# Kernel optimization log

Hardware: AMD Instinct MI355X
Metric: run time of the kernel (lower is better)

## Reference

```python
import jax, jax.numpy as jnp
import numpy as np

WD, WH, WW = 2, 7, 7
N = WD * WH * WW            # 98 tokens per window
C = 192                     # dim
H = 6                       # num_heads
HD = C // H                 # head_dim = 32
NW = 512                    # number of windows per sample
B = 4                       # batch
B_ = B * NW                 # 2048 windows total
TABLE = (2 * WD - 1) * (2 * WH - 1) * (2 * WW - 1)  # 507


def _relative_position_index():
    d, h, w = np.meshgrid(np.arange(WD), np.arange(WH), np.arange(WW), indexing='ij')
    coords = np.stack([d, h, w]).reshape(3, -1)              # (3, N)
    rel = coords[:, :, None] - coords[:, None, :]            # (3, N, N)
    rel = rel.transpose(1, 2, 0).astype(np.int64)            # (N, N, 3)
    rel[:, :, 0] += WD - 1
    rel[:, :, 1] += WH - 1
    rel[:, :, 2] += WW - 1
    rel[:, :, 0] *= (2 * WH - 1) * (2 * WW - 1)
    rel[:, :, 1] *= 2 * WW - 1
    return jnp.asarray(rel.sum(-1), dtype=jnp.int32)         # (N, N)


def setup_inputs() -> dict:
    key = jax.random.key(0)
    ks = jax.random.split(key, 7)
    return {
        'x': jax.random.normal(ks[0], (B_, N, C), dtype=jnp.float32),
        'mask': jax.random.normal(ks[1], (NW, N, N), dtype=jnp.float32),
        'qkv_w': jax.random.normal(ks[2], (3 * C, C), dtype=jnp.float32) * 0.02,
        'qkv_b': jnp.zeros((3 * C,), dtype=jnp.float32),
        'proj_w': jax.random.normal(ks[3], (C, C), dtype=jnp.float32) * 0.02,
        'proj_b': jnp.zeros((C,), dtype=jnp.float32),
        'rpb_table': jax.random.normal(ks[4], (TABLE, H), dtype=jnp.float32) * 0.02,
        'rel_pos_index': _relative_position_index(),
    }


def reference(x, mask, qkv_w, qkv_b, proj_w, proj_b, rpb_table, rel_pos_index):
    Bw, n, c = x.shape
    hd = c // H
    scale = hd ** -0.5
    qkv = (x @ qkv_w.T + qkv_b).reshape(Bw, n, 3, H, hd)
    q, k, v = qkv[:, :, 0], qkv[:, :, 1], qkv[:, :, 2]       # (Bw, n, H, hd)
    # attn = (q @ k^T) * scale  (scale applied after matmul, as in source)
    attn = jnp.einsum('bihd,bjhd->bhij', q, k) * scale       # (Bw, H, n, n)
    bias = rpb_table[rel_pos_index]                          # (n, n, H)
    attn = attn + jnp.transpose(bias, (2, 0, 1))[None]       # broadcast over Bw
    nw = mask.shape[0]
    attn = attn.reshape(Bw // nw, nw, H, n, n) + mask[None, :, None]
    attn = jax.nn.softmax(attn.reshape(Bw, H, n, n), axis=-1)
    out = jnp.einsum('bhij,bjhd->bihd', attn, v).reshape(Bw, n, c)
    return out @ proj_w.T + proj_b
```

## Files before the change

### kernel.cpp

```cpp
#include <hip/hip_runtime.h>
#include <hip/hip_bf16.h>

using bf16   = __bf16;
using bf16x4 = __attribute__((ext_vector_type(4))) __bf16;
using bf16x8 = __attribute__((ext_vector_type(8))) __bf16;
using f32x4  = __attribute__((ext_vector_type(4))) float;

#define B_TOT 2048
#define NTOK  98
#define CDIM  192
#define NHEAD 6
#define HDIM  32
#define NWIN  512
#define NN    (NTOK*NTOK)
#define QKV_ELEMS ((size_t)B_TOT*NHEAD*NTOK*HDIM)
#define MROWS 200704
#define SCALE 0.17677669529663687f

#define MFMA(a,b,c) __builtin_amdgcn_mfma_f32_16x16x32_bf16((a),(b),(c),0,0,0)

#define GLD16(gp, lp) __builtin_amdgcn_global_load_lds(                        \
    (const __attribute__((address_space(1))) void*)(gp),                       \
    (__attribute__((address_space(3))) void*)(lp), 16, 0, 0)

__global__ void build_bias(const float* __restrict__ table,
                           const int* __restrict__ rel,
                           float* __restrict__ bias) {
    int t = blockIdx.x * 256 + threadIdx.x;
    if (t < NN) {
        int idx = rel[t];
        #pragma unroll
        for (int h = 0; h < NHEAD; ++h)
            bias[h * NN + t] = table[idx * NHEAD + h];
    }
}

__global__ void conv_swz(const float* __restrict__ src, bf16* __restrict__ dst,
                         int nchunk) {
    int t = blockIdx.x * 256 + threadIdx.x;
    if (t < nchunk) {
        int row = t / 24, c = t % 24;
        const float* s = src + (size_t)row * CDIM + c * 8;
        bf16x8 o;
        #pragma unroll
        for (int e = 0; e < 8; ++e) o[e] = (bf16)s[e];
        *(bf16x8*)(dst + (size_t)row * CDIM + ((c ^ (row & 7)) << 3)) = o;
    }
}

__global__ __launch_bounds__(256) void qkv_gemm(
    const float* __restrict__ x, const bf16* __restrict__ wb,
    const float* __restrict__ bvec,
    bf16* __restrict__ qdst, bf16* __restrict__ kdst, bf16* __restrict__ vdst)
{
    __shared__ char Bs[2][24576];
    const int tid = threadIdx.x, lane = tid & 63, wv = tid >> 6;
    const int l15 = lane & 15, l16 = lane >> 4;
    const int m0 = blockIdx.x * 64;

    {
        const char* bsrc = (const char*)wb;
        #pragma unroll
        for (int j = 0; j < 6; ++j) {
            const int ch = wv * 6 + j;
            GLD16(bsrc + ch * 1024 + lane * 16, Bs[0] + ch * 1024);
        }
    }

    const int arow = wv * 16 + l15;
    const int grow = m0 + arow;
    const float* xr = x + (size_t)grow * CDIM + l16 * 8;
    bf16x8 af[6];
    #pragma unroll
    for (int ks = 0; ks < 6; ++ks) {
        float4 v0 = *(const float4*)(xr + ks * 32);
        float4 v1 = *(const float4*)(xr + ks * 32 + 4);
        bf16x8 a;
        a[0] = (bf16)v0.x; a[1] = (bf16)v0.y; a[2] = (bf16)v0.z; a[3] = (bf16)v0.w;
        a[4] = (bf16)v1.x; a[5] = (bf16)v1.y; a[6] = (bf16)v1.z; a[7] = (bf16)v1.w;
        af[ks] = a;
    }

    __syncthreads();

    const int rowoff = (grow / NTOK) * 18816 + (grow % NTOK) * 32;
    const f32x4 z4 = {0.f, 0.f, 0.f, 0.f};

    #pragma unroll
    for (int nc = 0; nc < 9; ++nc) {
        if (nc < 8) {
            const char* bsrc = (const char*)wb + (size_t)(nc + 1) * 24576;
            #pragma unroll
            for (int j = 0; j < 6; ++j) {
                const int ch = wv * 6 + j;
                GLD16(bsrc + ch * 1024 + lane * 16, Bs[(nc + 1) & 1] + ch * 1024);
            }
        }

        f32x4 acc[4];
        #pragma unroll
        for (int ct = 0; ct < 4; ++ct) acc[ct] = z4;

        #pragma unroll
        for (int ks = 0; ks < 6; ++ks) {
            #pragma unroll
            for (int ct = 0; ct < 4; ++ct) {
                const int brow = ct * 16 + l15;
                bf16x8 bf = *(const bf16x8*)(Bs[nc & 1] + brow * 384
                                             + (((ks * 4 + l16) ^ (brow & 7)) << 4));
                acc[ct] = MFMA(bf, af[ks], acc[ct]);
            }
        }

        #pragma unroll
        for (int ct = 0; ct < 4; ++ct) {
            const int g0    = nc * 64 + ct * 16;
            const int which = g0 / CDIM;
            const int cm    = g0 % CDIM;
            const int h     = cm >> 5, hd0 = cm & 31;
            const float4 bvf = *(const float4*)(bvec + g0 + l16 * 4);
            bf16x4 s;
            #pragma unroll
            for (int r = 0; r < 4; ++r) {
                float v = acc[ct][r] + ((const float*)&bvf)[r];
                if (which == 0) v *= SCALE;
                s[r] = (bf16)v;
            }
            bf16* dp = (which == 0) ? qdst : (which == 1) ? kdst : vdst;
            *(bf16x4*)(dp + rowoff + h * 3136 + hd0 + l16 * 4) = s;
        }
        __syncthreads();
    }
}

__global__ __launch_bounds__(256) void attn_fused(
    const bf16* __restrict__ q, const bf16* __restrict__ k,
    const bf16* __restrict__ v,
    const float* __restrict__ mask, const float* __restrict__ bias,
    bf16* __restrict__ ao)
{
    __shared__ char lds[4 * 8192 + 4 * 4096 + 4 * 64];
    const int tid = threadIdx.x, lane = tid & 63, wv = tid >> 6;
    const int l15 = lane & 15, l16 = lane >> 4;
    char*  Vt   = lds + wv * 8192;
    char*  P    = lds + 32768 + wv * 4096;
    float* invS = (float*)(lds + 49152 + wv * 64);

    const int u = blockIdx.x * 4 + wv;
    const int b = u / NHEAD, h = u - b * NHEAD;
    const int w = b & (NWIN - 1);
    const size_t bho = (size_t)u * 3136;

    bf16x8 vvv[7];
    #pragma unroll
    for (int t = 0; t < 7; ++t) {
        int idx = t * 64 + lane;
        int n = idx >> 2; if (n > 97) n = 97;
        int hd0 = (idx & 3) * 8;
        vvv[t] = *(const bf16x8*)(v + bho + n * 32 + hd0);
    }

    bf16x8 kf[7];
    #pragma unroll
    for (int jt = 0; jt < 7; ++jt) {
        int kr = jt * 16 + l15; if (kr > 97) kr = 97;
        kf[jt] = *(const bf16x8*)(k + bho + kr * HDIM + l16 * 8);
    }

    #pragma unroll
    for (int t = 0; t < 7; ++t) {
        int idx = t * 64 + lane;
        if (idx < 392) {
            int n = idx >> 2, hd0 = (idx & 3) * 8;
            #pragma unroll
            for (int e = 0; e < 8; ++e) {
                int hd = hd0 + e;
                *(bf16*)(Vt + hd * 256 + (((n >> 3) ^ (hd & 7)) << 4) + ((n & 7) << 1))
                    = vvv[t][e];
            }
        }
    }
    #pragma unroll
    for (int t = 0; t < 15; ++t) {
        int idx = t * 64 + lane;
        int hd = idx / 30, n = 98 + idx % 30;
        *(bf16*)(Vt + hd * 256 + (((n >> 3) ^ (hd & 7)) << 4) + ((n & 7) << 1)) = (bf16)0.f;
    }
    {
        int zr = lane >> 2;
        int zc = 112 + (lane & 3) * 4;
        *(unsigned long long*)(P + zr * 256 + (((zc >> 3) ^ (zr & 7)) << 4)
                               + ((zc & 7) << 1)) = 0ull;
    }

    const float* mrow = mask + (size_t)w * NN;
    const float* brow = bias + (size_t)h * NN;
    bf16* dst = ao + (size_t)b * NTOK * CDIM;
    const f32x4 z4 = {0.f, 0.f, 0.f, 0.f};

    #pragma unroll 1
    for (int it = 0; it < 7; ++it) {
        int qrow = it * 16 + l15; if (qrow > 97) qrow = 97;
        const bf16x8 qf = *(const bf16x8*)(q + bho + qrow * HDIM + l16 * 8);
        f32x4 acc[7];
        __builtin_amdgcn_s_setprio(1);
        #pragma unroll
        for (int jt = 0; jt < 7; ++jt)
            acc[jt] = MFMA(qf, kf[jt], z4);
        __builtin_amdgcn_s_setprio(0);

        #pragma unroll
        for (int r = 0; r < 4; ++r) {
            int i = it * 16 + l16 * 4 + r; if (i > 97) i = 97;
            float s = 0.f;
            #pragma unroll
            for (int jt = 0; jt < 7; ++jt) {
                int j = jt * 16 + l15;
                float mbv = (j < NTOK) ? (mrow[i * NTOK + j] + brow[i * NTOK + j])
                                       : -__builtin_inff();
                float e = __expf(acc[jt][r] + mbv);
                acc[jt][r] = e; s += e;
            }
            s += __shfl_xor(s, 1, 16);
            s += __shfl_xor(s, 2, 16);
            s += __shfl_xor(s, 4, 16);
            s += __shfl_xor(s, 8, 16);
            if (l15 == 0) invS[l16 * 4 + r] = 1.f / s;
        }

        #pragma unroll
        for (int jt = 0; jt < 7; ++jt) {
            #pragma unroll
            for (int r = 0; r < 4; ++r) {
                int row = l16 * 4 + r;
                int j = jt * 16 + l15;
                *(bf16*)(P + row * 256 + (((j >> 3) ^ (row & 7)) << 4) + ((j & 7) << 1))
                    = (bf16)acc[jt][r];
            }
        }

        f32x4 o0 = z4, o1 = z4;
        __builtin_amdgcn_s_setprio(1);
        #pragma unroll
        for (int ks = 0; ks < 4; ++ks) {
            int kchunk = ks * 4 + l16;
            bf16x8 pf = *(const bf16x8*)(P + l15 * 256 + ((kchunk ^ (l15 & 7)) << 4));
            bf16x8 v0 = *(const bf16x8*)(Vt + l15 * 256 + ((kchunk ^ (l15 & 7)) << 4));
            bf16x8 v1 = *(const bf16x8*)(Vt + (16 + l15) * 256 + ((kchunk ^ (l15 & 7)) << 4));
            o0 = MFMA(v0, pf, o0);
            o1 = MFMA(v1, pf, o1);
        }
        __builtin_amdgcn_s_setprio(0);

        {
            int row = it * 16 + l15;
            if (row < NTOK) {
                float inv = invS[l15];
                bf16x4 s0, s1;
                #pragma unroll
                for (int r = 0; r < 4; ++r) {
                    s0[r] = (bf16)(o0[r] * inv);
                    s1[r] = (bf16)(o1[r] * inv);
                }
                const int swr = (b * NTOK + row) & 7;
                const int c0 = h * 4 + (l16 >> 1);
                const int c1 = c0 + 2;
                const int wi = (l16 & 1) << 2;
                *(bf16x4*)(dst + (size_t)row * CDIM + (((c0 ^ swr) << 3) | wi)) = s0;
                *(bf16x4*)(dst + (size_t)row * CDIM + (((c1 ^ swr) << 3) | wi)) = s1;
            }
        }
    }
}

__global__ __launch_bounds__(256) void proj_gemm(
    const bf16* __restrict__ ao, const bf16* __restrict__ wb,
    const float* __restrict__ bvec, float* __restrict__ out)
{
    __shared__ char As[24576];
    __shared__ char Bs[2][24576];
    const int tid = threadIdx.x, lane = tid & 63, wv = tid >> 6;
    const int l15 = lane & 15, l16 = lane >> 4;
    const int m0 = blockIdx.x * 64;

    {
        const char* asrc = (const char*)ao + (size_t)m0 * 384;
        const char* bsrc = (const char*)wb;
        #pragma unroll
        for (int j = 0; j < 6; ++j) {
            const int ch = wv * 6 + j;
            GLD16(asrc + ch * 1024 + lane * 16, As + ch * 1024);
            GLD16(bsrc + ch * 1024 + lane * 16, Bs[0] + ch * 1024);
        }
    }
    __syncthreads();

    const int arow = wv * 16 + l15;
    bf16x8 af[6];
    #pragma unroll
    for (int ks = 0; ks < 6; ++ks)
        af[ks] = *(const bf16x8*)(As + arow * 384 + (((ks * 4 + l16) ^ (arow & 7)) << 4));

    const size_t orow = (size_t)(m0 + arow) * CDIM;
    const f32x4 z4 = {0.f, 0.f, 0.f, 0.f};

    #pragma unroll
    for (int nc = 0; nc < 3; ++nc) {
        if (nc < 2) {
            const char* bsrc = (const char*)wb + (size_t)(nc + 1) * 24576;
            #pragma unroll
            for (int j = 0; j < 6; ++j) {
                const int ch = wv * 6 + j;
                GLD16(bsrc + ch * 1024 + lane * 16, Bs[(nc + 1) & 1] + ch * 1024);
            }
        }

        f32x4 acc[4];
        #pragma unroll
        for (int ct = 0; ct < 4; ++ct) acc[ct] = z4;

        #pragma unroll
        for (int ks = 0; ks < 6; ++ks) {
            #pragma unroll
            for (int ct = 0; ct < 4; ++ct) {
                const int brow = ct * 16 + l15;
                bf16x8 bf = *(const bf16x8*)(Bs[nc & 1] + brow * 384
                                             + (((ks * 4 + l16) ^ (brow & 7)) << 4));
                acc[ct] = MFMA(bf, af[ks], acc[ct]);
            }
        }

        #pragma unroll
        for (int ct = 0; ct < 4; ++ct) {
            const int g0 = nc * 64 + ct * 16;
            const float4 bvf = *(const float4*)(bvec + g0 + l16 * 4);
            f32x4 s;
            #pragma unroll
            for (int r = 0; r < 4; ++r)
                s[r] = acc[ct][r] + ((const float*)&bvf)[r];
            *(f32x4*)(out + orow + g0 + l16 * 4) = s;
        }
        __syncthreads();
    }
}

extern "C" void kernel_launch(void* const* d_in, const int* in_sizes, int n_in,
                              void* d_out, int out_size, void* d_ws, size_t ws_size,
                              hipStream_t stream)
{
    (void)in_sizes; (void)n_in; (void)out_size; (void)ws_size;
    const float* x      = (const float*)d_in[0];
    const float* mask   = (const float*)d_in[1];
    const float* qkv_w  = (const float*)d_in[2];
    const float* qkv_b  = (const float*)d_in[3];
    const float* proj_w = (const float*)d_in[4];
    const float* proj_b = (const float*)d_in[5];
    const float* rpb    = (const float*)d_in[6];
    const int*   rel    = (const int*)d_in[7];
    float* out = (float*)d_out;

    char* ws = (char*)d_ws;
    bf16* qb = (bf16*)ws;
    bf16* kb = qb + QKV_ELEMS;
    bf16* vb = kb + QKV_ELEMS;
    size_t off = 3 * QKV_ELEMS * sizeof(bf16);
    float* bias = (float*)(ws + off);
    off += ((size_t)NHEAD * NN * 4 + 255) / 256 * 256;
    bf16* ao = (bf16*)(ws + off);
    bf16* qwb = ao;
    bf16* pwb = qb;

    build_bias<<<(NN + 255) / 256, 256, 0, stream>>>(rpb, rel, bias);
    conv_swz<<<(576 * 24 + 255) / 256, 256, 0, stream>>>(qkv_w, qwb, 576 * 24);
    qkv_gemm<<<MROWS / 64, 256, 0, stream>>>(x, qwb, qkv_b, qb, kb, vb);
    attn_fused<<<(B_TOT * NHEAD) / 4, 256, 0, stream>>>(qb, kb, vb, mask, bias, ao);
    conv_swz<<<(192 * 24 + 255) / 256, 256, 0, stream>>>(proj_w, pwb, 192 * 24);
    proj_gemm<<<MROWS / 64, 256, 0, stream>>>(ao, pwb, proj_b, out);
}
```

Measured before the change: 330.1 us.

## Precombine mask and bias into padded bf16 table and prefetch next tile

Adds a kernel that folds the window mask and relative-position bias into one padded bf16 table per (window, head), stored temporarily in the output buffer. The attention kernel then reads one bf16 value per score instead of two fp32 loads, with no bounds checks. It also software-pipelines the next query fragment and mask tile into registers while the current tile computes. In exchange there is an extra pre-pass kernel, more register pressure, and bf16 rounding of the combined mask and bias.

```diff
diff --git a/kernel.cpp b/kernel.cpp
--- a/kernel.cpp
+++ b/kernel.cpp
@@ -15,6 +15,7 @@
 #define NN    (NTOK*NTOK)
 #define QKV_ELEMS ((size_t)B_TOT*NHEAD*NTOK*HDIM)
 #define MROWS 200704
+#define MBCU  12544
 #define SCALE 0.17677669529663687f
 
 #define MFMA(a,b,c) __builtin_amdgcn_mfma_f32_16x16x32_bf16((a),(b),(c),0,0,0)
@@ -32,6 +33,26 @@
         #pragma unroll
         for (int h = 0; h < NHEAD; ++h)
             bias[h * NN + t] = table[idx * NHEAD + h];
+    }
+}
+
+__global__ void build_mbc(const float* __restrict__ mask,
+                          const float* __restrict__ bias,
+                          bf16* __restrict__ mbc) {
+    const int u = blockIdx.x;
+    const int w = u / NHEAD, h = u - w * NHEAD;
+    const float* mrow = mask + (size_t)w * NN;
+    const float* brow = bias + (size_t)h * NN;
+    bf16* dst = mbc + (size_t)u * MBCU;
+    for (int e = threadIdx.x; e < MBCU; e += 256) {
+        int i = e / 112, j = e - i * 112;
+        float val;
+        if (i < NTOK)
+            val = (j < NTOK) ? (mrow[i * NTOK + j] + brow[i * NTOK + j])
+                             : -__builtin_inff();
+        else
+            val = 0.f;
+        dst[e] = (bf16)val;
     }
 }
 
@@ -136,7 +157,7 @@
 __global__ __launch_bounds__(256) void attn_fused(
     const bf16* __restrict__ q, const bf16* __restrict__ k,
     const bf16* __restrict__ v,
-    const float* __restrict__ mask, const float* __restrict__ bias,
+    const bf16* __restrict__ mbc,
     bf16* __restrict__ ao)
 {
     __shared__ char lds[4 * 8192 + 4 * 4096 + 4 * 64];
@@ -150,6 +171,7 @@
     const int b = u / NHEAD, h = u - b * NHEAD;
     const int w = b & (NWIN - 1);
     const size_t bho = (size_t)u * 3136;
+    const bf16* mbu = mbc + (size_t)(w * NHEAD + h) * MBCU;
 
     bf16x8 vvv[7];
     #pragma unroll
@@ -193,32 +215,48 @@
                                + ((zc & 7) << 1)) = 0ull;
     }
 
-    const float* mrow = mask + (size_t)w * NN;
-    const float* brow = bias + (size_t)h * NN;
     bf16* dst = ao + (size_t)b * NTOK * CDIM;
     const f32x4 z4 = {0.f, 0.f, 0.f, 0.f};
 
+    bf16x8 qfC;
+    bf16   mbC[7][4];
+    {
+        qfC = *(const bf16x8*)(q + bho + l15 * HDIM + l16 * 8);
+        #pragma unroll
+        for (int jt = 0; jt < 7; ++jt)
+            #pragma unroll
+            for (int r = 0; r < 4; ++r)
+                mbC[jt][r] = mbu[(l16 * 4 + r) * 112 + jt * 16 + l15];
+    }
+
     #pragma unroll 1
     for (int it = 0; it < 7; ++it) {
-        int qrow = it * 16 + l15; if (qrow > 97) qrow = 97;
-        const bf16x8 qf = *(const bf16x8*)(q + bho + qrow * HDIM + l16 * 8);
+        bf16x8 qfN;
+        bf16   mbN[7][4];
+        if (it < 6) {
+            int qrow2 = (it + 1) * 16 + l15; if (qrow2 > 97) qrow2 = 97;
+            qfN = *(const bf16x8*)(q + bho + qrow2 * HDIM + l16 * 8);
+            const bf16* mrow = mbu + ((it + 1) * 16) * 112;
+            #pragma unroll
+            for (int jt = 0; jt < 7; ++jt)
+                #pragma unroll
+                for (int r = 0; r < 4; ++r)
+                    mbN[jt][r] = mrow[(l16 * 4 + r) * 112 + jt * 16 + l15];
+        }
+
         f32x4 acc[7];
         __builtin_amdgcn_s_setprio(1);
         #pragma unroll
         for (int jt = 0; jt < 7; ++jt)
-            acc[jt] = MFMA(qf, kf[jt], z4);
+            acc[jt] = MFMA(qfC, kf[jt], z4);
         __builtin_amdgcn_s_setprio(0);
 
         #pragma unroll
         for (int r = 0; r < 4; ++r) {
-            int i = it * 16 + l16 * 4 + r; if (i > 97) i = 97;
             float s = 0.f;
             #pragma unroll
             for (int jt = 0; jt < 7; ++jt) {
-                int j = jt * 16 + l15;
-                float mbv = (j < NTOK) ? (mrow[i * NTOK + j] + brow[i * NTOK + j])
-                                       : -__builtin_inff();
-                float e = __expf(acc[jt][r] + mbv);
+                float e = __expf(acc[jt][r] + (float)mbC[jt][r]);
                 acc[jt][r] = e; s += e;
             }
             s += __shfl_xor(s, 1, 16);
@@ -270,6 +308,15 @@
                 *(bf16x4*)(dst + (size_t)row * CDIM + (((c1 ^ swr) << 3) | wi)) = s1;
             }
         }
+
+        if (it < 6) {
+            qfC = qfN;
+            #pragma unroll
+            for (int jt = 0; jt < 7; ++jt)
+                #pragma unroll
+                for (int r = 0; r < 4; ++r)
+                    mbC[jt][r] = mbN[jt][r];
+        }
     }
 }
 
@@ -369,11 +416,13 @@
     bf16* ao = (bf16*)(ws + off);
     bf16* qwb = ao;
     bf16* pwb = qb;
+    bf16* mbc = (bf16*)d_out;
 
     build_bias<<<(NN + 255) / 256, 256, 0, stream>>>(rpb, rel, bias);
+    build_mbc<<<NWIN * NHEAD, 256, 0, stream>>>(mask, bias, mbc);
     conv_swz<<<(576 * 24 + 255) / 256, 256, 0, stream>>>(qkv_w, qwb, 576 * 24);
     qkv_gemm<<<MROWS / 64, 256, 0, stream>>>(x, qwb, qkv_b, qb, kb, vb);
-    attn_fused<<<(B_TOT * NHEAD) / 4, 256, 0, stream>>>(qb, kb, vb, mask, bias, ao);
+    attn_fused<<<(B_TOT * NHEAD) / 4, 256, 0, stream>>>(qb, kb, vb, mbc, ao);
     conv_swz<<<(192 * 24 + 255) / 256, 256, 0, stream>>>(proj_w, pwb, 192 * 24);
     proj_gemm<<<MROWS / 64, 256, 0, stream>>>(ao, pwb, proj_b, out);
 }
```

Result: slower. 366.8 us (+11.1%).
